# Performance work log

Measured on AMD Instinct MI355X. Metric: run time of the kernel, lower is better.

Reference implementation:

```python
import jax, jax.numpy as jnp
import numpy as np

HEAD_DIM = 128


def block_causal_mask(cu_seqlens, seq_len, dtype):
    # positions -> which packed document each token belongs to
    positions = jnp.arange(seq_len)
    seq_ids = jnp.searchsorted(cu_seqlens, positions, side='right') - 1
    same_seq = seq_ids[:, None] == seq_ids[None, :]
    causal = positions[None, :] <= positions[:, None]  # key_pos <= query_pos
    neg_inf = jnp.asarray(float('-inf'), dtype)
    return jnp.where(same_seq & causal, jnp.asarray(0.0, dtype), neg_inf)


def setup_inputs() -> dict:
    key = jax.random.key(0)
    kq, kk, kv = jax.random.split(key, 3)
    B, H, S, D = 1, 8, 4096, HEAD_DIM
    q = jax.random.normal(kq, (B, H, S, D), dtype=jnp.float32)
    k = jax.random.normal(kk, (B, H, S, D), dtype=jnp.float32)
    v = jax.random.normal(kv, (B, H, S, D), dtype=jnp.float32)
    # 4 packed documents of length 1024 each; cu_seqlens[-1] == seq_len
    cu_seqlens = jnp.array([0, 1024, 2048, 3072, 4096], dtype=jnp.int32)
    return {"q": q, "k": k, "v": v, "cu_seqlens": cu_seqlens, "max_seqlen": 1024}


def reference(q, k, v, cu_seqlens, max_seqlen):
    seq_len = q.shape[2]
    scale = 1.0 / jnp.sqrt(jnp.asarray(q.shape[-1], q.dtype))
    mask = block_causal_mask(cu_seqlens, seq_len, q.dtype)  # [S, S]
    # scores: [B, H, Sq, Sk]
    scores = jnp.einsum('bhqd,bhkd->bhqk', q, k) * scale + mask
    probs = jax.nn.softmax(scores, axis=-1)
    return jnp.einsum('bhqk,bhkd->bhqd', probs, v)
```

## Files before the change

### kernel.cpp

```cpp
#include <hip/hip_runtime.h>
#include <hip/hip_bf16.h>


#define HD 128
#define BR 64
#define BC 128

typedef __attribute__((ext_vector_type(8))) short short8;
typedef __attribute__((ext_vector_type(4))) float floatx4;

__device__ inline unsigned packbf2(float lo, float hi) {
    __hip_bfloat162 h2 = __float22bfloat162_rn(make_float2(lo, hi));
    return *reinterpret_cast<unsigned*>(&h2);
}
__device__ inline short bfs(float f) {
    __hip_bfloat16 b = __float2bfloat16(f);
    return *reinterpret_cast<short*>(&b);
}

__device__ inline void gll16(const void* g, void* l) {
    __builtin_amdgcn_global_load_lds(
        (const __attribute__((address_space(1))) unsigned int*)g,
        (__attribute__((address_space(3))) unsigned int*)l, 16, 0, 0);
}

__global__ __launch_bounds__(256) void prepack(
    const float* __restrict__ K, const float* __restrict__ V,
    unsigned short* __restrict__ wsK, unsigned short* __restrict__ wsVT,
    int S)
{
    const int tid = threadIdx.x;
    const int nVblk = 8 * (S >> 6);
    const int bid = blockIdx.x;
    if (bid < nVblk) {
        __shared__ __align__(8) unsigned short sV[HD * 68];
        const int ntile = S >> 6;
        const int h = bid / ntile;
        const int t = bid - h * ntile;
        const float* vb = V + ((size_t)h * S + t * 64) * HD;
        {
            const int rp = tid >> 3;
            const int dc = tid & 7;
            const int r0 = rp * 2;
            const int d0 = dc * 16;
            const float* p0 = vb + (size_t)r0 * HD + d0;
            const float* p1 = p0 + HD;
            float4 a0 = *(const float4*)(p0 + 0),  a1 = *(const float4*)(p0 + 4);
            float4 a2 = *(const float4*)(p0 + 8),  a3 = *(const float4*)(p0 + 12);
            float4 b0 = *(const float4*)(p1 + 0),  b1 = *(const float4*)(p1 + 4);
            float4 b2 = *(const float4*)(p1 + 8),  b3 = *(const float4*)(p1 + 12);
            float av[16] = {a0.x,a0.y,a0.z,a0.w, a1.x,a1.y,a1.z,a1.w,
                            a2.x,a2.y,a2.z,a2.w, a3.x,a3.y,a3.z,a3.w};
            float bv[16] = {b0.x,b0.y,b0.z,b0.w, b1.x,b1.y,b1.z,b1.w,
                            b2.x,b2.y,b2.z,b2.w, b3.x,b3.y,b3.z,b3.w};
            #pragma unroll
            for (int i = 0; i < 16; ++i) {
                unsigned pr = packbf2(av[i], bv[i]);
                *(unsigned*)((char*)sV + ((size_t)(d0 + i) * 68 + r0) * 2) = pr;
            }
        }
        __syncthreads();
        const int d  = tid >> 1;
        const int jj = tid & 1;
        char* dstrow = (char*)wsVT + (((size_t)(h * ntile + t) * HD + d) * 128);
        const int dx = (d & 7) << 4;
        const unsigned short* srow = sV + (size_t)d * 68;
        #pragma unroll
        for (int u = 0; u < 4; ++u) {
            const int j  = jj * 4 + u;
            const int k0 = (j >> 2) * 32 + (j & 3) * 4;
            uint2 lo = *(const uint2*)(srow + k0);
            uint2 hi = *(const uint2*)(srow + k0 + 16);
            uint4 w = make_uint4(lo.x, lo.y, hi.x, hi.y);
            *(uint4*)(dstrow + ((j * 16) ^ dx)) = w;
        }
    } else {
        const int cid = (bid - nVblk) * 256 + tid;
        const int row = cid >> 4;
        const int c   = cid & 15;
        const float* src = K + (size_t)row * HD + c * 8;
        float4 f0 = *(const float4*)src;
        float4 f1 = *(const float4*)(src + 4);
        union { uint4 q; unsigned u[4]; } w;
        w.u[0] = packbf2(f0.x, f0.y); w.u[1] = packbf2(f0.z, f0.w);
        w.u[2] = packbf2(f1.x, f1.y); w.u[3] = packbf2(f1.z, f1.w);
        *(uint4*)((char*)wsK + (size_t)row * 256 + ((c * 16) ^ ((row & 7) << 4))) = w.q;
    }
}

__global__ __launch_bounds__(512, 1) void fa_fwd(
    const float* __restrict__ Q,
    const unsigned short* __restrict__ wsK,
    const unsigned short* __restrict__ wsVT,
    const int* __restrict__ cu_seqlens, int n_cu,
    float* __restrict__ O,
    int S)
{
    __shared__ alignas(16) __hip_bfloat16 sK2[2][BC * HD];
    __shared__ alignas(16) unsigned int   sVT2[2][2 * HD * 32];

    const int tid  = threadIdx.x;
    const int wave = tid >> 6;
    const int gp   = wave >> 2;
    const int wsub = wave & 3;
    const int lane = tid & 63;
    const int quad = lane >> 4;
    const int l16  = lane & 15;
    const int kx   = (l16 & 7) << 4;

    const int nqb = S / BR;
    const int h   = blockIdx.x & 7;
    const int g   = (int)(blockIdx.x >> 3);
    int qb;
    if (nqb == 64) {
        qb = (g & 3) * 16 + (15 - (g >> 2));
    } else {
        qb = nqb - 1 - g;
    }
    const int q0    = qb * BR;
    const int qw    = q0 + wsub * 16;
    const int qlane = qw + l16;

    int blk_ds = 0;
    for (int i = 0; i < n_cu; ++i) {
        int c = cu_seqlens[i];
        if (c <= q0) blk_ds = c;
    }
    const int k_begin = blk_ds & ~(BC - 1);
    const int ntiles  = (q0 + BR - 1 - k_begin) / BC + 1;

    const char* gkb = (const char*)wsK + (size_t)h * S * 256;
    const char* gvb = (const char*)wsVT + (size_t)h * (S >> 6) * 16384;
    const int wofs = (wave & 3) * 8192;
    const int lo = wofs + lane * 16;
    auto stage = [&](int kt, int buf) {
        if (gp == 0) {
            const char* gk = gkb + (size_t)kt * 256 + lo;
            char* lk = (char*)&sK2[buf][0] + wofs;
            #pragma unroll
            for (int c = 0; c < 8; ++c) gll16(gk + c * 1024, lk + c * 1024);
        } else {
            const char* gv = gvb + (size_t)(kt >> 6) * 16384 + lo;
            char* lv = (char*)&sVT2[buf][0] + wofs;
            #pragma unroll
            for (int c = 0; c < 8; ++c) gll16(gv + c * 1024, lv + c * 1024);
        }
    };

    const size_t hoff = (size_t)h * S * HD;
    const float* Qh = Q + hoff;
    float*       Oh = O + hoff;

    short8 aq[4];
    {
        const float* qp = Qh + (size_t)qlane * HD + quad * 8;
        #pragma unroll
        for (int ks = 0; ks < 4; ++ks) {
            float4 a0 = *(const float4*)(qp + ks * 32);
            float4 a1 = *(const float4*)(qp + ks * 32 + 4);
            short8 a;
            a[0] = bfs(a0.x); a[1] = bfs(a0.y); a[2] = bfs(a0.z); a[3] = bfs(a0.w);
            a[4] = bfs(a1.x); a[5] = bfs(a1.y); a[6] = bfs(a1.z); a[7] = bfs(a1.w);
            aq[ks] = a;
        }
    }

    int ds_lane = 0;
    for (int i = 0; i < n_cu; ++i) {
        int c = cu_seqlens[i];
        if (c <= qlane) ds_lane = c;
    }

    stage(k_begin, 0);

    floatx4 oacc[8];
    #pragma unroll
    for (int dt = 0; dt < 8; ++dt) oacc[dt] = (floatx4){0.f, 0.f, 0.f, 0.f};
    float m_r = -1e30f, l_r = 0.f;

    const float sl = 0.08838834764831845f * 1.4426950408889634f;

    for (int it = 0; it < ntiles; ++it) {
        const int kt  = k_begin + it * BC;
        const int buf = it & 1;

        asm volatile("s_waitcnt vmcnt(0)\n\ts_barrier" ::: "memory");

        if (it + 1 < ntiles) stage(kt + BC, buf ^ 1);

        if (kt + gp * 64 <= qw + 15) {
            const char* kbase = (const char*)&sK2[buf][0];
            const char* vbase = (const char*)&sVT2[buf][0] + gp * 16384;

            floatx4 sc[4];
            __builtin_amdgcn_s_setprio(1);
            #pragma unroll
            for (int ctl = 0; ctl < 4; ++ctl) {
                if (kt + gp * 64 + ctl * 16 <= qw + 15) {
                    floatx4 c = (floatx4){0.f, 0.f, 0.f, 0.f};
                    #pragma unroll
                    for (int ks = 0; ks < 4; ++ks) {
                        short8 a = *(const short8*)(kbase
                            + (gp * 64 + ctl * 16 + l16) * 256
                            + (((ks * 4 + quad) << 4) ^ kx));
                        c = __builtin_amdgcn_mfma_f32_16x16x32_bf16(a, aq[ks], c, 0, 0, 0);
                    }
                    sc[ctl] = c;
                } else {
                    sc[ctl] = (floatx4){-1e30f, -1e30f, -1e30f, -1e30f};
                }
            }
            __builtin_amdgcn_s_setprio(0);

            #pragma unroll
            for (int ctl = 0; ctl < 4; ++ctl) {
                if (kt + gp * 64 + ctl * 16 <= qw + 15) {
                    #pragma unroll
                    for (int r = 0; r < 4; ++r) {
                        const int key = kt + gp * 64 + ctl * 16 + quad * 4 + r;
                        const bool valid = (key <= qlane) && (key >= ds_lane);
                        float s = sc[ctl][r] * sl;
                        sc[ctl][r] = valid ? s : -1e30f;
                    }
                }
            }

            float mx01 = fmaxf(fmaxf(fmaxf(sc[0][0], sc[0][1]), fmaxf(sc[0][2], sc[0][3])),
                               fmaxf(fmaxf(sc[1][0], sc[1][1]), fmaxf(sc[1][2], sc[1][3])));
            float mx23 = fmaxf(fmaxf(fmaxf(sc[2][0], sc[2][1]), fmaxf(sc[2][2], sc[2][3])),
                               fmaxf(fmaxf(sc[3][0], sc[3][1]), fmaxf(sc[3][2], sc[3][3])));
            float mx = fmaxf(mx01, mx23);
            mx = fmaxf(mx, __shfl_xor(mx, 16, 64));
            mx = fmaxf(mx, __shfl_xor(mx, 32, 64));

            if (__any(mx > m_r + 8.f)) {
                const float mnew = fmaxf(m_r, mx);
                const float al   = exp2f(m_r - mnew);
                m_r = mnew;
                l_r *= al;
                #pragma unroll
                for (int dt = 0; dt < 8; ++dt) {
                    #pragma unroll
                    for (int r = 0; r < 4; ++r)
                        oacc[dt][r] *= al;
                }
            }
            const float live = (m_r > -1e29f) ? 1.f : 0.f;

            float ssum = 0.f;
            #pragma unroll
            for (int ctl = 0; ctl < 4; ++ctl) {
                #pragma unroll
                for (int r = 0; r < 4; ++r) {
                    float p = exp2f(sc[ctl][r] - m_r) * live;
                    sc[ctl][r] = p;
                    ssum += p;
                }
            }
            l_r += ssum;

            __builtin_amdgcn_s_setprio(1);
            #pragma unroll
            for (int ks = 0; ks < 2; ++ks) {
                if (kt + gp * 64 + ks * 32 <= qw + 15) {
                    union { unsigned u[4]; short8 s; } pu;
                    pu.u[0] = packbf2(sc[2*ks][0],   sc[2*ks][1]);
                    pu.u[1] = packbf2(sc[2*ks][2],   sc[2*ks][3]);
                    pu.u[2] = packbf2(sc[2*ks+1][0], sc[2*ks+1][1]);
                    pu.u[3] = packbf2(sc[2*ks+1][2], sc[2*ks+1][3]);
                    #pragma unroll
                    for (int dt = 0; dt < 8; ++dt) {
                        union { uint4 q; short8 s; } cv;
                        cv.q = *(const uint4*)(vbase + (dt * 16 + l16) * 128
                                               + (((ks * 4 + quad) << 4) ^ kx));
                        oacc[dt] = __builtin_amdgcn_mfma_f32_16x16x32_bf16(cv.s, pu.s, oacc[dt], 0, 0, 0);
                    }
                }
            }
            __builtin_amdgcn_s_setprio(0);
        }
    }

    l_r += __shfl_xor(l_r, 16, 64);
    l_r += __shfl_xor(l_r, 32, 64);

    __syncthreads();

    float* obuf = (float*)&sK2[0][0];
    float* lbuf = (float*)&sVT2[0][0];
    if (gp == 1) {
        float* ob = obuf + wsub * 2048;
        #pragma unroll
        for (int dt = 0; dt < 8; ++dt) {
            const int sw = (dt ^ (lane & 7)) << 2;
            float4 st;
            st.x = oacc[dt][0]; st.y = oacc[dt][1];
            st.z = oacc[dt][2]; st.w = oacc[dt][3];
            *(float4*)(ob + lane * 32 + sw) = st;
        }
        if (quad == 0) {
            lbuf[wsub * 128 + l16]      = m_r;
            lbuf[wsub * 128 + 64 + l16] = l_r;
        }
    }
    __syncthreads();
    if (gp == 0) {
        const float m2 = lbuf[wsub * 128 + l16];
        const float l2 = lbuf[wsub * 128 + 64 + l16];
        const float M  = fmaxf(m_r, m2);
        const float w1 = exp2f(m_r - M);
        const float w2 = exp2f(m2 - M);
        const float inv = 1.0f / (w1 * l_r + w2 * l2);
        const float* ob = obuf + wsub * 2048;
        float* op = Oh + (size_t)qlane * HD + quad * 4;
        #pragma unroll
        for (int dt = 0; dt < 8; ++dt) {
            const int sw = (dt ^ (lane & 7)) << 2;
            float4 o2 = *(const float4*)(ob + lane * 32 + sw);
            float4 st;
            st.x = (w1 * oacc[dt][0] + w2 * o2.x) * inv;
            st.y = (w1 * oacc[dt][1] + w2 * o2.y) * inv;
            st.z = (w1 * oacc[dt][2] + w2 * o2.z) * inv;
            st.w = (w1 * oacc[dt][3] + w2 * o2.w) * inv;
            *(float4*)(op + dt * 16) = st;
        }
    }
}

extern "C" void kernel_launch(void* const* d_in, const int* in_sizes, int n_in,
                              void* d_out, int out_size, void* d_ws, size_t ws_size,
                              hipStream_t stream) {
    const float* q = (const float*)d_in[0];
    const float* k = (const float*)d_in[1];
    const float* v = (const float*)d_in[2];
    const int* cu = (const int*)d_in[3];
    const int n_cu = in_sizes[3];
    const int H = 8;
    const int S = in_sizes[0] / (H * HD);
    float* out = (float*)d_out;

    const int nqb = S / BR;
    unsigned short* wsK  = (unsigned short*)d_ws;
    unsigned short* wsVT = wsK + (size_t)H * S * HD;

    const int nVblk = H * (S >> 6);
    const int nKblk = (H * S) / 16;
    prepack<<<dim3(nVblk + nKblk), dim3(256), 0, stream>>>(k, v, wsK, wsVT, S);

    dim3 grid(H * nqb);
    dim3 block(512);
    fa_fwd<<<grid, block, 0, stream>>>(q, wsK, wsVT, cu, n_cu, out, S);
}
```

Baseline: 126.5 us.

## Fold softmax scale into Q, skip interior masking, use native exp2

The softmax scale and log2e factor are now multiplied into Q before the bf16 conversion, which removes a per-score multiply in the inner loop. Masking is skipped for 16-key column tiles that are fully valid, meaning entirely causal and inside the current document. exp2f is replaced by the hardware exp2 builtin, which drops the range-handling wrapper. The prepack block-to-head mapping is also reordered so heads interleave across blocks. Scaling Q before rounding to bf16 changes the rounding slightly, and the native exp2 has reduced denormal handling.

```diff
diff --git a/kernel.cpp b/kernel.cpp
--- a/kernel.cpp
+++ b/kernel.cpp
@@ -17,6 +17,7 @@
     __hip_bfloat16 b = __float2bfloat16(f);
     return *reinterpret_cast<short*>(&b);
 }
+__device__ inline float fexp2(float x) { return __builtin_amdgcn_exp2f(x); }
 
 __device__ inline void gll16(const void* g, void* l) {
     __builtin_amdgcn_global_load_lds(
@@ -35,8 +36,8 @@
     if (bid < nVblk) {
         __shared__ __align__(8) unsigned short sV[HD * 68];
         const int ntile = S >> 6;
-        const int h = bid / ntile;
-        const int t = bid - h * ntile;
+        const int h = bid & 7;
+        const int t = bid >> 3;
         const float* vb = V + ((size_t)h * S + t * 64) * HD;
         {
             const int rp = tid >> 3;
@@ -75,16 +76,20 @@
             *(uint4*)(dstrow + ((j * 16) ^ dx)) = w;
         }
     } else {
-        const int cid = (bid - nVblk) * 256 + tid;
-        const int row = cid >> 4;
-        const int c   = cid & 15;
-        const float* src = K + (size_t)row * HD + c * 8;
+        const int b2  = bid - nVblk;
+        const int h   = b2 & 7;
+        const int idx = b2 >> 3;
+        const int cid = idx * 256 + tid;
+        const int rowh = cid >> 4;
+        const int c    = cid & 15;
+        const size_t row = (size_t)h * S + rowh;
+        const float* src = K + row * HD + c * 8;
         float4 f0 = *(const float4*)src;
         float4 f1 = *(const float4*)(src + 4);
         union { uint4 q; unsigned u[4]; } w;
         w.u[0] = packbf2(f0.x, f0.y); w.u[1] = packbf2(f0.z, f0.w);
         w.u[2] = packbf2(f1.x, f1.y); w.u[3] = packbf2(f1.z, f1.w);
-        *(uint4*)((char*)wsK + (size_t)row * 256 + ((c * 16) ^ ((row & 7) << 4))) = w.q;
+        *(uint4*)((char*)wsK + row * 256 + ((c * 16) ^ ((rowh & 7) << 4))) = w.q;
     }
 }
 
@@ -112,11 +117,8 @@
     const int h   = blockIdx.x & 7;
     const int g   = (int)(blockIdx.x >> 3);
     int qb;
-    if (nqb == 64) {
-        qb = (g & 3) * 16 + (15 - (g >> 2));
-    } else {
-        qb = nqb - 1 - g;
-    }
+    if (nqb == 64) qb = (g & 3) * 16 + (15 - (g >> 2));
+    else           qb = nqb - 1 - g;
     const int q0    = qb * BR;
     const int qw    = q0 + wsub * 16;
     const int qlane = qw + l16;
@@ -151,6 +153,7 @@
     const float* Qh = Q + hoff;
     float*       Oh = O + hoff;
 
+    const float sl = 0.08838834764831845f * 1.4426950408889634f;
     short8 aq[4];
     {
         const float* qp = Qh + (size_t)qlane * HD + quad * 8;
@@ -159,8 +162,10 @@
             float4 a0 = *(const float4*)(qp + ks * 32);
             float4 a1 = *(const float4*)(qp + ks * 32 + 4);
             short8 a;
-            a[0] = bfs(a0.x); a[1] = bfs(a0.y); a[2] = bfs(a0.z); a[3] = bfs(a0.w);
-            a[4] = bfs(a1.x); a[5] = bfs(a1.y); a[6] = bfs(a1.z); a[7] = bfs(a1.w);
+            a[0] = bfs(a0.x * sl); a[1] = bfs(a0.y * sl);
+            a[2] = bfs(a0.z * sl); a[3] = bfs(a0.w * sl);
+            a[4] = bfs(a1.x * sl); a[5] = bfs(a1.y * sl);
+            a[6] = bfs(a1.z * sl); a[7] = bfs(a1.w * sl);
             aq[ks] = a;
         }
     }
@@ -178,14 +183,11 @@
     for (int dt = 0; dt < 8; ++dt) oacc[dt] = (floatx4){0.f, 0.f, 0.f, 0.f};
     float m_r = -1e30f, l_r = 0.f;
 
-    const float sl = 0.08838834764831845f * 1.4426950408889634f;
-
     for (int it = 0; it < ntiles; ++it) {
         const int kt  = k_begin + it * BC;
         const int buf = it & 1;
 
         asm volatile("s_waitcnt vmcnt(0)\n\ts_barrier" ::: "memory");
-
         if (it + 1 < ntiles) stage(kt + BC, buf ^ 1);
 
         if (kt + gp * 64 <= qw + 15) {
@@ -214,13 +216,13 @@
 
             #pragma unroll
             for (int ctl = 0; ctl < 4; ++ctl) {
-                if (kt + gp * 64 + ctl * 16 <= qw + 15) {
+                const int kc = kt + gp * 64 + ctl * 16;
+                if (kc <= qw + 15 && !(kc + 15 <= qw && kc >= blk_ds)) {
                     #pragma unroll
                     for (int r = 0; r < 4; ++r) {
-                        const int key = kt + gp * 64 + ctl * 16 + quad * 4 + r;
+                        const int key = kc + quad * 4 + r;
                         const bool valid = (key <= qlane) && (key >= ds_lane);
-                        float s = sc[ctl][r] * sl;
-                        sc[ctl][r] = valid ? s : -1e30f;
+                        sc[ctl][r] = valid ? sc[ctl][r] : -1e30f;
                     }
                 }
             }
@@ -235,7 +237,7 @@
 
             if (__any(mx > m_r + 8.f)) {
                 const float mnew = fmaxf(m_r, mx);
-                const float al   = exp2f(m_r - mnew);
+                const float al   = fexp2(m_r - mnew);
                 m_r = mnew;
                 l_r *= al;
                 #pragma unroll
@@ -252,7 +254,7 @@
             for (int ctl = 0; ctl < 4; ++ctl) {
                 #pragma unroll
                 for (int r = 0; r < 4; ++r) {
-                    float p = exp2f(sc[ctl][r] - m_r) * live;
+                    float p = fexp2(sc[ctl][r] - m_r) * live;
                     sc[ctl][r] = p;
                     ssum += p;
                 }
@@ -308,8 +310,8 @@
         const float m2 = lbuf[wsub * 128 + l16];
         const float l2 = lbuf[wsub * 128 + 64 + l16];
         const float M  = fmaxf(m_r, m2);
-        const float w1 = exp2f(m_r - M);
-        const float w2 = exp2f(m2 - M);
+        const float w1 = fexp2(m_r - M);
+        const float w2 = fexp2(m2 - M);
         const float inv = 1.0f / (w1 * l_r + w2 * l2);
         const float* ob = obuf + wsub * 2048;
         float* op = Oh + (size_t)qlane * HD + quad * 4;
```

Measured after the change: 124.0 us. No clear change (-2.0%).
